# Kernel optimization log

Hardware: AMD Instinct MI355X
Metric: run time of the kernel (lower is better)

Reference implementation:

```python
import jax, jax.numpy as jnp
import numpy as np

DIM, IDIM, HEADS = 256, 64, 4
B, I, J = 1, 256, 256
EPS = 1e-5


def _sinu(seq, rot):
    inv = 1.0 / (10000.0 ** (np.arange(0, rot, 2, dtype=np.float64) / rot))
    f = np.arange(seq, dtype=np.float64)[:, None] * inv[None, :]   # [seq, rot/2]
    f = np.repeat(f, 2, axis=-1)                                   # [seq, rot]
    return (jnp.asarray(np.sin(f)[None], dtype=jnp.float32),
            jnp.asarray(np.cos(f)[None], dtype=jnp.float32))       # [1, seq, rot]


def setup_inputs() -> dict:
    key = jax.random.key(0)
    ks = jax.random.split(key, 8)
    w = DIM ** -0.5
    sin_i, cos_i = _sinu(J, IDIM)
    sin_j, cos_j = _sinu(I, IDIM)
    return {
        'x': jax.random.normal(ks[0], (B, I, J, DIM), jnp.float32),
        'sin_i': sin_i, 'cos_i': cos_i, 'sin_j': sin_j, 'cos_j': cos_j,
        'gia': jnp.ones((DIM,), jnp.float32), 'bia': jnp.zeros((DIM,), jnp.float32),
        'gib': jnp.ones((DIM,), jnp.float32), 'bib': jnp.zeros((DIM,), jnp.float32),
        'Wq_i': jax.random.normal(ks[1], (DIM, IDIM * HEADS), jnp.float32) * w,
        'Wkv_i': jax.random.normal(ks[2], (DIM, 2 * IDIM * HEADS), jnp.float32) * w,
        'Wo_i': jax.random.normal(ks[3], (IDIM * HEADS, DIM), jnp.float32) * w,
        'bo_i': jnp.zeros((DIM,), jnp.float32),
        'gja': jnp.ones((DIM,), jnp.float32), 'bja': jnp.zeros((DIM,), jnp.float32),
        'gjb': jnp.ones((DIM,), jnp.float32), 'bjb': jnp.zeros((DIM,), jnp.float32),
        'Wq_j': jax.random.normal(ks[4], (DIM, IDIM * HEADS), jnp.float32) * w,
        'Wkv_j': jax.random.normal(ks[5], (DIM, 2 * IDIM * HEADS), jnp.float32) * w,
        'Wo_j': jax.random.normal(ks[6], (IDIM * HEADS, DIM), jnp.float32) * w,
        'bo_j': jnp.zeros((DIM,), jnp.float32),
    }


def _ln(x, g, b):
    mu = jnp.mean(x, axis=-1, keepdims=True)
    var = jnp.mean((x - mu) ** 2, axis=-1, keepdims=True)
    return (x - mu) / jnp.sqrt(var + EPS) * g + b


def _rotate_every_two(x):
    x1, x2 = x[..., ::2], x[..., 1::2]
    return jnp.stack((-x2, x1), axis=-1).reshape(x.shape)


def _rope(x, sin, cos):
    # sin/cos: [1, seq, rot] -> [1, 1, seq, rot] (broadcast over heads)
    sin, cos = sin[:, None], cos[:, None]
    rd = sin.shape[-1]
    xr, xp = x[..., :rd], x[..., rd:]
    xr = xr * cos + _rotate_every_two(xr) * sin
    return jnp.concatenate((xr, xp), axis=-1)


def _attn(a, sin, cos, ga, ba, gb, bb, Wq, Wkv, Wo, bo):
    an = _ln(a, ga, ba)
    bn = _ln(a, gb, bb)  # a == b in axial use
    q = an @ Wq
    k, v = jnp.split(bn @ Wkv, 2, axis=-1)
    Bn, N = a.shape[0], a.shape[1]
    def heads(t):
        return t.reshape(Bn, N, HEADS, IDIM).transpose(0, 2, 1, 3)  # b h n d
    q, k, v = heads(q), heads(k), heads(v)
    q = _rope(q, sin, cos)
    k = _rope(k, sin, cos)
    dots = jnp.einsum('bhid,bhjd->bhij', q, k)  # scale = 1 (as in source)
    attn = jax.nn.softmax(dots, axis=-1)
    out = jnp.einsum('bhij,bhjd->bhid', attn, v)
    out = out.transpose(0, 2, 3, 1).reshape(Bn, N, IDIM * HEADS)  # 'b h i d -> b i (d h)'
    return jax.nn.elu(out @ Wo + bo)


def reference(x, sin_i, cos_i, sin_j, cos_j,
              gia, bia, gib, bib, Wq_i, Wkv_i, Wo_i, bo_i,
              gja, bja, gjb, bjb, Wq_j, Wkv_j, Wo_j, bo_j):
    b, i, j, d = x.shape
    xi = x.reshape(b * i, j, d)
    xi = _attn(xi, sin_i, cos_i, gia, bia, gib, bib, Wq_i, Wkv_i, Wo_i, bo_i)
    xi = xi.reshape(b, i, j, d)
    xj = x.transpose(0, 2, 1, 3).reshape(b * j, i, d)
    xj = _attn(xj, sin_j, cos_j, gja, bja, gjb, bjb, Wq_j, Wkv_j, Wo_j, bo_j)
    xj = xj.reshape(b, j, i, d).transpose(0, 2, 1, 3)
    return x + (xi + xj) / 2
```

## Files before the change

### kernel.cpp

```cpp
#include <hip/hip_runtime.h>
#include <math.h>

#define DIM    256
#define IDIM   64
#define HEADS  4
#define NSEQ   256
#define SEQLEN 256
#define NTOK   (NSEQ * SEQLEN)
#define EPSLN  1e-5f

typedef __attribute__((ext_vector_type(8))) short bf16x8s;
typedef __attribute__((ext_vector_type(4))) float f32x4;

union BF8 { bf16x8s v; unsigned short u[8]; };

__device__ __forceinline__ float bf2f(unsigned short u) {
    union { unsigned int i; float f; } v; v.i = ((unsigned int)u) << 16; return v.f;
}
__device__ __forceinline__ unsigned short f2bf(float f) {
    union { float f; unsigned int i; } v; v.f = f;
    unsigned int x = v.i;
    return (unsigned short)((x + 0x7fffu + ((x >> 16) & 1u)) >> 16);
}

__device__ bf16x8s g_wpk[8][8192];

__global__ __launch_bounds__(256) void wpack_all_kernel(
    const float* __restrict__ Wq_i, const float* __restrict__ Wkv_i,
    const float* __restrict__ Wo_i,
    const float* __restrict__ Wq_j, const float* __restrict__ Wkv_j,
    const float* __restrict__ Wo_j)
{
    const int slot = blockIdx.y;
    const int pass = slot >> 2, m = slot & 3;
    const float* W; int ldw, col0, perm;
    if (m == 0)      { W = pass ? Wq_j  : Wq_i;  ldw = 256; col0 = 0;   perm = 0; }
    else if (m == 1) { W = pass ? Wkv_j : Wkv_i; ldw = 512; col0 = 0;   perm = 0; }
    else if (m == 2) { W = pass ? Wkv_j : Wkv_i; ldw = 512; col0 = 256; perm = 0; }
    else             { W = pass ? Wo_j  : Wo_i;  ldw = 256; col0 = 0;   perm = 1; }

    const int gtile = blockIdx.x * 4 + (threadIdx.x >> 6);
    const int l = threadIdx.x & 63;
    const int nt = gtile >> 3, kt = gtile & 7;
    const int n = nt * 16 + (l & 15);
    const int k0 = kt * 32 + (l >> 4) * 8;
    BF8 o;
#pragma unroll
    for (int j = 0; j < 8; ++j) {
        int k = k0 + j;
        int src = perm ? ((k & 63) * 4 + (k >> 6)) : k;
        o.u[j] = f2bf(W[(size_t)src * ldw + col0 + n]);
    }
    g_wpk[slot][(size_t)gtile * 64 + l] = o.v;
}

#define XLD  264
#define GOFF (32 * XLD)
#define CLD2 261

__global__ __launch_bounds__(512) void lnqkv_kernel(
    const float* __restrict__ x,
    const float* __restrict__ sin_t, const float* __restrict__ cos_t,
    const float* __restrict__ ga, const float* __restrict__ ba,
    const float* __restrict__ gb, const float* __restrict__ bb,
    bf16x8s* __restrict__ qo, bf16x8s* __restrict__ ko, bf16x8s* __restrict__ vo,
    int pass)
{
    __shared__ float smf[32 * XLD + 1024];

    const int tid = threadIdx.x;
    const int l = tid & 63, w = tid >> 6;
    const int lr = l & 15, lk = l >> 4;
    const int t0 = blockIdx.x * 32;
    const int seq = t0 >> 8;
    const int pos0 = t0 & 255;
    const int wbase = pass * 4;

    {
        const int half = tid >> 8;
        const int col  = tid & 255;
        for (int rr = 0; rr < 16; ++rr) {
            int r = rr + 16 * half;
            int t = t0 + r;
            int row = (pass == 0) ? t : ((t & 255) * NSEQ + (t >> 8));
            smf[r * XLD + col] = x[(size_t)row * DIM + col];
        }
        smf[GOFF + tid]       = (tid < 256) ? ga[tid] : ba[tid - 256];
        smf[GOFF + 512 + tid] = (tid < 256) ? gb[tid] : bb[tid - 256];
    }
    __syncthreads();

    {
        const int r = tid >> 4, sub = tid & 15;
        float s1 = 0.f, s2 = 0.f;
        for (int m = 0; m < 16; ++m) { float v = smf[r * XLD + sub + 16 * m]; s1 += v; s2 += v * v; }
        for (int off = 1; off < 16; off <<= 1) {
            s1 += __shfl_xor(s1, off, 64);
            s2 += __shfl_xor(s2, off, 64);
        }
        float mu = s1 * (1.f / 256.f);
        float var = s2 * (1.f / 256.f) - mu * mu;
        float rstd = rsqrtf(var + EPSLN);
        for (int m = 0; m < 16; ++m) {
            int d = sub + 16 * m;
            smf[r * XLD + d] = (smf[r * XLD + d] - mu) * rstd;
        }
    }
    __syncthreads();

    f32x4 acc[2][6];
#pragma unroll
    for (int mf = 0; mf < 2; ++mf)
#pragma unroll
        for (int nf = 0; nf < 6; ++nf) { f32x4 z = {0.f, 0.f, 0.f, 0.f}; acc[mf][nf] = z; }

    const int nt0 = w * 6;
    const bool needA = (nt0 < 16);
    const bool needB = (nt0 + 5 >= 16);

    for (int ks = 0; ks < 8; ++ks) {
        const int c0 = ks * 32 + lk * 8;
        if (needA) {
            BF8 ah[2], al[2];
#pragma unroll
            for (int mf = 0; mf < 2; ++mf) {
                const float* xr = &smf[(mf * 16 + lr) * XLD + c0];
                const float* gg = &smf[GOFF + c0];
                const float* bv = &smf[GOFF + 256 + c0];
#pragma unroll
                for (int j = 0; j < 8; ++j) {
                    float a = xr[j] * gg[j] + bv[j];
                    unsigned short hi = f2bf(a);
                    ah[mf].u[j] = hi;
                    al[mf].u[j] = f2bf(a - bf2f(hi));
                }
            }
#pragma unroll
            for (int nf = 0; nf < 6; ++nf) {
                int ntg = nt0 + nf;
                if (ntg < 16) {
                    const bf16x8s b = g_wpk[wbase][((size_t)(ntg * 8 + ks)) * 64 + l];
#pragma unroll
                    for (int mf = 0; mf < 2; ++mf) {
                        acc[mf][nf] = __builtin_amdgcn_mfma_f32_16x16x32_bf16(al[mf].v, b, acc[mf][nf], 0, 0, 0);
                        acc[mf][nf] = __builtin_amdgcn_mfma_f32_16x16x32_bf16(ah[mf].v, b, acc[mf][nf], 0, 0, 0);
                    }
                }
            }
        }
        if (needB) {
            BF8 ah[2], al[2];
#pragma unroll
            for (int mf = 0; mf < 2; ++mf) {
                const float* xr = &smf[(mf * 16 + lr) * XLD + c0];
                const float* gg = &smf[GOFF + 512 + c0];
                const float* bv = &smf[GOFF + 768 + c0];
#pragma unroll
                for (int j = 0; j < 8; ++j) {
                    float a = xr[j] * gg[j] + bv[j];
                    unsigned short hi = f2bf(a);
                    ah[mf].u[j] = hi;
                    al[mf].u[j] = f2bf(a - bf2f(hi));
                }
            }
#pragma unroll
            for (int nf = 0; nf < 6; ++nf) {
                int ntg = nt0 + nf;
                if (ntg >= 16) {
                    const bf16x8s b = g_wpk[wbase + (ntg >> 4)][((size_t)((ntg & 15) * 8 + ks)) * 64 + l];
#pragma unroll
                    for (int mf = 0; mf < 2; ++mf) {
                        acc[mf][nf] = __builtin_amdgcn_mfma_f32_16x16x32_bf16(al[mf].v, b, acc[mf][nf], 0, 0, 0);
                        acc[mf][nf] = __builtin_amdgcn_mfma_f32_16x16x32_bf16(ah[mf].v, b, acc[mf][nf], 0, 0, 0);
                    }
                }
            }
        }
    }
    __syncthreads();

    for (int c = 0; c < 3; ++c) {
#pragma unroll
        for (int nf = 0; nf < 6; ++nf) {
            int ntg = nt0 + nf;
            if ((ntg >> 4) == c) {
                int cb = (ntg & 15) * 16 + lr;
#pragma unroll
                for (int mf = 0; mf < 2; ++mf)
#pragma unroll
                    for (int r = 0; r < 4; ++r)
                        smf[(mf * 16 + lk * 4 + r) * CLD2 + cb] = acc[mf][nf][r];
            }
        }
        __syncthreads();

        if (c < 2) {
#pragma unroll
            for (int p = 0; p < 2; ++p) {
                int tile = w * 2 + p;
                int h = tile >> 2, mt = (tile >> 1) & 1, ktd = tile & 1;
                int row = mt * 16 + lr;
                int pos = pos0 + row;
                int d0 = ktd * 32 + lk * 8;
                const float* src = &smf[row * CLD2 + h * 64 + d0];
                BF8 o;
#pragma unroll
                for (int p2 = 0; p2 < 4; ++p2) {
                    float cs = cos_t[pos * IDIM + d0 + 2 * p2];
                    float sn = sin_t[pos * IDIM + d0 + 2 * p2];
                    float e = src[2 * p2], od = src[2 * p2 + 1];
                    o.u[2 * p2]     = f2bf(e * cs - od * sn);
                    o.u[2 * p2 + 1] = f2bf(od * cs + e * sn);
                }
                int sh = seq * 4 + h;
                int mtg = (pos0 >> 4) + mt;
                bf16x8s* dst = c ? ko : qo;
                dst[((size_t)sh * 32 + mtg * 2 + ktd) * 64 + l] = o.v;
            }
        } else {
#pragma unroll
            for (int p = 0; p < 2; ++p) {
                int tile = w * 2 + p;
                int h = tile >> 2, ntd = tile & 3;
                BF8 o;
#pragma unroll
                for (int j = 0; j < 8; ++j)
                    o.u[j] = f2bf(smf[(lk * 8 + j) * CLD2 + h * 64 + ntd * 16 + lr]);
                int sh = seq * 4 + h;
                int ktg = pos0 >> 5;
                vo[((size_t)sh * 32 + ktg * 4 + ntd) * 64 + l] = o.v;
            }
        }
        __syncthreads();
    }
}

__global__ __launch_bounds__(256) void attn_kernel(
    const bf16x8s* __restrict__ qpk, const bf16x8s* __restrict__ kpk,
    const bf16x8s* __restrict__ vpk, bf16x8s* __restrict__ opk)
{
    __shared__ __align__(16) unsigned short Pus[4 * 64 * 64];
    char* Pb = (char*)Pus;
    const int tid = threadIdx.x, l = tid & 63, w = tid >> 6;
    const int lr = l & 15, lk = l >> 4;
    const int sh = blockIdx.x;
    const size_t base = (size_t)sh * 32 * 64;

    bf16x8s qf[4][2];
#pragma unroll
    for (int mf = 0; mf < 4; ++mf)
#pragma unroll
        for (int kt = 0; kt < 2; ++kt)
            qf[mf][kt] = qpk[base + ((size_t)((w * 4 + mf) * 2 + kt)) * 64 + l];

    f32x4 O[4][4];
    float mrun[4][4], lrun[4][4];
#pragma unroll
    for (int mf = 0; mf < 4; ++mf)
#pragma unroll
        for (int nf = 0; nf < 4; ++nf) { f32x4 z = {0.f, 0.f, 0.f, 0.f}; O[mf][nf] = z; }
#pragma unroll
    for (int mf = 0; mf < 4; ++mf)
#pragma unroll
        for (int r = 0; r < 4; ++r) { mrun[mf][r] = -1e30f; lrun[mf][r] = 0.f; }

    for (int ktk = 0; ktk < 4; ++ktk) {
        f32x4 S[4][4];
#pragma unroll
        for (int mf = 0; mf < 4; ++mf)
#pragma unroll
            for (int nf = 0; nf < 4; ++nf) { f32x4 z = {0.f, 0.f, 0.f, 0.f}; S[mf][nf] = z; }
#pragma unroll
        for (int ks = 0; ks < 2; ++ks) {
            bf16x8s kf[4];
#pragma unroll
            for (int nf = 0; nf < 4; ++nf)
                kf[nf] = kpk[base + ((size_t)((ktk * 4 + nf) * 2 + ks)) * 64 + l];
#pragma unroll
            for (int mf = 0; mf < 4; ++mf)
#pragma unroll
                for (int nf = 0; nf < 4; ++nf)
                    S[mf][nf] = __builtin_amdgcn_mfma_f32_16x16x32_bf16(qf[mf][ks], kf[nf], S[mf][nf], 0, 0, 0);
        }
#pragma unroll
        for (int mf = 0; mf < 4; ++mf) {
#pragma unroll
            for (int r = 0; r < 4; ++r) {
                float mt_ = fmaxf(fmaxf(S[mf][0][r], S[mf][1][r]), fmaxf(S[mf][2][r], S[mf][3][r]));
                for (int off = 1; off < 16; off <<= 1) mt_ = fmaxf(mt_, __shfl_xor(mt_, off, 64));
                float mnew = fmaxf(mrun[mf][r], mt_);
                float sc = __expf(mrun[mf][r] - mnew);
#pragma unroll
                for (int nf = 0; nf < 4; ++nf) O[mf][nf][r] *= sc;
                float ps = 0.f;
#pragma unroll
                for (int nf = 0; nf < 4; ++nf) {
                    float pp = __expf(S[mf][nf][r] - mnew);
                    S[mf][nf][r] = pp;
                    ps += pp;
                }
                for (int off = 1; off < 16; off <<= 1) ps += __shfl_xor(ps, off, 64);
                lrun[mf][r] = lrun[mf][r] * sc + ps;
                mrun[mf][r] = mnew;
            }
        }
#pragma unroll
        for (int mf = 0; mf < 4; ++mf)
#pragma unroll
            for (int nf = 0; nf < 4; ++nf)
#pragma unroll
                for (int r = 0; r < 4; ++r) {
                    int row = mf * 16 + lk * 4 + r, col = nf * 16 + lr;
                    unsigned int byte = ((unsigned)((w * 64 + row) * 64 + col) * 2) ^ (unsigned)((row & 7) << 4);
                    *(unsigned short*)(Pb + byte) = f2bf(S[mf][nf][r]);
                }
        __syncthreads();
#pragma unroll
        for (int ks = 0; ks < 2; ++ks) {
            bf16x8s vf[4];
#pragma unroll
            for (int nf = 0; nf < 4; ++nf)
                vf[nf] = vpk[base + ((size_t)((ktk * 2 + ks) * 4 + nf)) * 64 + l];
#pragma unroll
            for (int mf = 0; mf < 4; ++mf) {
                int row = mf * 16 + lr;
                unsigned int byte = ((unsigned)((w * 64 + row) * 64 + ks * 32 + lk * 8) * 2) ^ (unsigned)((row & 7) << 4);
                bf16x8s pa = *(const bf16x8s*)(Pb + byte);
#pragma unroll
                for (int nf = 0; nf < 4; ++nf)
                    O[mf][nf] = __builtin_amdgcn_mfma_f32_16x16x32_bf16(pa, vf[nf], O[mf][nf], 0, 0, 0);
            }
        }
        __syncthreads();
    }

#pragma unroll
    for (int mf = 0; mf < 4; ++mf)
#pragma unroll
        for (int r = 0; r < 4; ++r) {
            float inv = 1.f / lrun[mf][r];
#pragma unroll
            for (int nf = 0; nf < 4; ++nf) {
                int row = mf * 16 + lk * 4 + r, col = nf * 16 + lr;
                unsigned int byte = ((unsigned)((w * 64 + row) * 64 + col) * 2) ^ (unsigned)((row & 7) << 4);
                *(unsigned short*)(Pb + byte) = f2bf(O[mf][nf][r] * inv);
            }
        }
    __syncthreads();
    const int seq = sh >> 2, h = sh & 3;
#pragma unroll
    for (int mf = 0; mf < 4; ++mf)
#pragma unroll
        for (int ktd = 0; ktd < 2; ++ktd) {
            int row = mf * 16 + lr;
            unsigned int byte = ((unsigned)((w * 64 + row) * 64 + ktd * 32 + lk * 8) * 2) ^ (unsigned)((row & 7) << 4);
            bf16x8s o = *(const bf16x8s*)(Pb + byte);
            size_t mtg = (size_t)seq * 16 + w * 4 + mf;
            opk[(mtg * 8 + h * 2 + ktd) * 64 + l] = o;
        }
}

__device__ __forceinline__ void gemm_core(
    const bf16x8s* __restrict__ A, const bf16x8s* __restrict__ B,
    int mt0, int nt0, int l, f32x4 acc[4][4])
{
#pragma unroll
    for (int mf = 0; mf < 4; ++mf)
#pragma unroll
        for (int nf = 0; nf < 4; ++nf) { f32x4 z = {0.f, 0.f, 0.f, 0.f}; acc[mf][nf] = z; }
#pragma unroll
    for (int ks = 0; ks < 8; ++ks) {
        bf16x8s a[4], b[4];
#pragma unroll
        for (int mf = 0; mf < 4; ++mf) a[mf] = A[((size_t)(mt0 + mf) * 8 + ks) * 64 + l];
#pragma unroll
        for (int nf = 0; nf < 4; ++nf) b[nf] = B[((size_t)(nt0 + nf) * 8 + ks) * 64 + l];
#pragma unroll
        for (int mf = 0; mf < 4; ++mf)
#pragma unroll
            for (int nf = 0; nf < 4; ++nf)
                acc[mf][nf] = __builtin_amdgcn_mfma_f32_16x16x32_bf16(a[mf], b[nf], acc[mf][nf], 0, 0, 0);
    }
}

__global__ __launch_bounds__(256) void gemm_proj_kernel(
    const bf16x8s* __restrict__ A,
    const float* __restrict__ x, const float* __restrict__ bo,
    float* __restrict__ out, int pass)
{
    __shared__ unsigned short Cus[128][136];
    const int tid = threadIdx.x;
    const int l = tid & 63, w = tid >> 6;
    const int wm = w >> 1, wn = w & 1;
    const int mb = blockIdx.x, nb = blockIdx.y;

    f32x4 acc[4][4];
    gemm_core(A, g_wpk[pass * 4 + 3], mb * 8 + wm * 4, nb * 8 + wn * 4, l, acc);

#pragma unroll
    for (int mf = 0; mf < 4; ++mf)
#pragma unroll
        for (int nf = 0; nf < 4; ++nf)
#pragma unroll
            for (int r = 0; r < 4; ++r)
                Cus[wm * 64 + mf * 16 + (l >> 4) * 4 + r][wn * 64 + nf * 16 + (l & 15)] =
                    f2bf(acc[mf][nf][r]);
    __syncthreads();

    const int row = tid >> 1;
    const int cc0 = (tid & 1) * 64;
    const int tok = mb * 128 + row;
    const size_t prow = (pass == 0) ? (size_t)tok
                                    : ((size_t)(tok & 255) * NSEQ + (tok >> 8));
    const size_t gb = prow * DIM + nb * 128 + cc0;
#pragma unroll
    for (int qq = 0; qq < 16; ++qq) {
        float4 r4;
        const float4 b4 = *reinterpret_cast<const float4*>(&bo[nb * 128 + cc0 + qq * 4]);
        float y0 = bf2f(Cus[row][cc0 + qq * 4 + 0]) + b4.x;
        float y1 = bf2f(Cus[row][cc0 + qq * 4 + 1]) + b4.y;
        float y2 = bf2f(Cus[row][cc0 + qq * 4 + 2]) + b4.z;
        float y3 = bf2f(Cus[row][cc0 + qq * 4 + 3]) + b4.w;
        r4.x = 0.5f * (y0 > 0.f ? y0 : expm1f(y0));
        r4.y = 0.5f * (y1 > 0.f ? y1 : expm1f(y1));
        r4.z = 0.5f * (y2 > 0.f ? y2 : expm1f(y2));
        r4.w = 0.5f * (y3 > 0.f ? y3 : expm1f(y3));
        if (pass == 0) {
            const float4 x4 = *reinterpret_cast<const float4*>(&x[gb + qq * 4]);
            r4.x += x4.x; r4.y += x4.y; r4.z += x4.z; r4.w += x4.w;
            *reinterpret_cast<float4*>(&out[gb + qq * 4]) = r4;
        } else {
            float4* op = reinterpret_cast<float4*>(&out[gb + qq * 4]);
            float4 o4 = *op;
            o4.x += r4.x; o4.y += r4.y; o4.z += r4.z; o4.w += r4.w;
            *op = o4;
        }
    }
}

extern "C" void kernel_launch(void* const* d_in, const int* in_sizes, int n_in,
                              void* d_out, int out_size, void* d_ws, size_t ws_size,
                              hipStream_t stream) {
    const float* x     = (const float*)d_in[0];
    const float* sin_i = (const float*)d_in[1];
    const float* cos_i = (const float*)d_in[2];
    const float* sin_j = (const float*)d_in[3];
    const float* cos_j = (const float*)d_in[4];
    const float* gia   = (const float*)d_in[5];
    const float* bia   = (const float*)d_in[6];
    const float* gib   = (const float*)d_in[7];
    const float* bib   = (const float*)d_in[8];
    const float* Wq_i  = (const float*)d_in[9];
    const float* Wkv_i = (const float*)d_in[10];
    const float* Wo_i  = (const float*)d_in[11];
    const float* bo_i  = (const float*)d_in[12];
    const float* gja   = (const float*)d_in[13];
    const float* bja   = (const float*)d_in[14];
    const float* gjb   = (const float*)d_in[15];
    const float* bjb   = (const float*)d_in[16];
    const float* Wq_j  = (const float*)d_in[17];
    const float* Wkv_j = (const float*)d_in[18];
    const float* Wo_j  = (const float*)d_in[19];
    const float* bo_j  = (const float*)d_in[20];

    float* out = (float*)d_out;

    char* base = (char*)d_ws;
    const size_t MB32 = 33554432;
    bf16x8s* buf0 = (bf16x8s*)(base);
    bf16x8s* buf1 = (bf16x8s*)(base + MB32);
    bf16x8s* buf2 = (bf16x8s*)(base + 2 * MB32);
    bf16x8s* buf3 = (bf16x8s*)(base + 3 * MB32);

    wpack_all_kernel<<<dim3(32, 8), 256, 0, stream>>>(Wq_i, Wkv_i, Wo_i, Wq_j, Wkv_j, Wo_j);

    for (int pass = 0; pass < 2; ++pass) {
        const float* sin_t = pass ? sin_j : sin_i;
        const float* cos_t = pass ? cos_j : cos_i;
        const float* ga = pass ? gja : gia;  const float* ba = pass ? bja : bia;
        const float* gb = pass ? gjb : gib;  const float* bb = pass ? bjb : bib;
        const float* bo = pass ? bo_j : bo_i;

        lnqkv_kernel<<<2048, 512, 0, stream>>>(
            x, sin_t, cos_t, ga, ba, gb, bb, buf2, buf3, buf0, pass);
        attn_kernel<<<1024, 256, 0, stream>>>(buf2, buf3, buf0, buf1);
        gemm_proj_kernel<<<dim3(512, 2), 256, 0, stream>>>(buf1, x, bo, out, pass);
    }
}
```

Before: 638.9 us.

## Fold LayerNorm affine into QKV weights and precompute bf16 hi/lo split once

Folds the LayerNorm gamma into the packed Q/KV weights and turns beta into a per-column bias (beta·W), computed once by a new small kernel and added in the epilogue. The normalized activations are split into bf16 hi/lo once per element and stored in shared memory, so the GEMM inner loop does vector LDS loads instead of per-fragment affine math and conversions. The two code paths for the A and B normalizations also merge into one. The trade-offs are an extra tiny kernel launch and a slightly different rounding order, since gamma is rounded into the bf16 weights.

```diff
diff --git a/kernel.cpp b/kernel.cpp
--- a/kernel.cpp
+++ b/kernel.cpp
@@ -24,20 +24,24 @@
 }
 
 __device__ bf16x8s g_wpk[8][8192];
+__device__ float g_bias[8][256];
 
 __global__ __launch_bounds__(256) void wpack_all_kernel(
     const float* __restrict__ Wq_i, const float* __restrict__ Wkv_i,
     const float* __restrict__ Wo_i,
     const float* __restrict__ Wq_j, const float* __restrict__ Wkv_j,
-    const float* __restrict__ Wo_j)
+    const float* __restrict__ Wo_j,
+    const float* __restrict__ gia, const float* __restrict__ gib,
+    const float* __restrict__ gja, const float* __restrict__ gjb)
 {
     const int slot = blockIdx.y;
     const int pass = slot >> 2, m = slot & 3;
     const float* W; int ldw, col0, perm;
-    if (m == 0)      { W = pass ? Wq_j  : Wq_i;  ldw = 256; col0 = 0;   perm = 0; }
-    else if (m == 1) { W = pass ? Wkv_j : Wkv_i; ldw = 512; col0 = 0;   perm = 0; }
-    else if (m == 2) { W = pass ? Wkv_j : Wkv_i; ldw = 512; col0 = 256; perm = 0; }
-    else             { W = pass ? Wo_j  : Wo_i;  ldw = 256; col0 = 0;   perm = 1; }
+    const float* gam;
+    if (m == 0)      { W = pass ? Wq_j  : Wq_i;  ldw = 256; col0 = 0;   perm = 0; gam = pass ? gja : gia; }
+    else if (m == 1) { W = pass ? Wkv_j : Wkv_i; ldw = 512; col0 = 0;   perm = 0; gam = pass ? gjb : gib; }
+    else if (m == 2) { W = pass ? Wkv_j : Wkv_i; ldw = 512; col0 = 256; perm = 0; gam = pass ? gjb : gib; }
+    else             { W = pass ? Wo_j  : Wo_i;  ldw = 256; col0 = 0;   perm = 1; gam = 0; }
 
     const int gtile = blockIdx.x * 4 + (threadIdx.x >> 6);
     const int l = threadIdx.x & 63;
@@ -49,24 +53,44 @@
     for (int j = 0; j < 8; ++j) {
         int k = k0 + j;
         int src = perm ? ((k & 63) * 4 + (k >> 6)) : k;
-        o.u[j] = f2bf(W[(size_t)src * ldw + col0 + n]);
+        float wv = W[(size_t)src * ldw + col0 + n];
+        if (gam) wv *= gam[k];
+        o.u[j] = f2bf(wv);
     }
     g_wpk[slot][(size_t)gtile * 64 + l] = o.v;
 }
 
+__global__ __launch_bounds__(256) void bias_kernel(
+    const float* __restrict__ bia, const float* __restrict__ bib,
+    const float* __restrict__ bja, const float* __restrict__ bjb,
+    const float* __restrict__ Wq_i, const float* __restrict__ Wkv_i,
+    const float* __restrict__ Wq_j, const float* __restrict__ Wkv_j)
+{
+    const int s = blockIdx.x;
+    const int pass = s / 3, m = s % 3;
+    const float* beta = (m == 0) ? (pass ? bja : bia) : (pass ? bjb : bib);
+    const float* W    = (m == 0) ? (pass ? Wq_j : Wq_i) : (pass ? Wkv_j : Wkv_i);
+    const int ldw  = (m == 0) ? 256 : 512;
+    const int col0 = (m == 2) ? 256 : 0;
+    const int col  = threadIdx.x;
+    float acc = 0.f;
+    for (int k = 0; k < 256; ++k) acc += beta[k] * W[(size_t)k * ldw + col0 + col];
+    g_bias[pass * 4 + m][col] = acc;
+}
+
 #define XLD  264
-#define GOFF (32 * XLD)
+#define HLD  264
 #define CLD2 261
 
 __global__ __launch_bounds__(512) void lnqkv_kernel(
     const float* __restrict__ x,
     const float* __restrict__ sin_t, const float* __restrict__ cos_t,
-    const float* __restrict__ ga, const float* __restrict__ ba,
-    const float* __restrict__ gb, const float* __restrict__ bb,
     bf16x8s* __restrict__ qo, bf16x8s* __restrict__ ko, bf16x8s* __restrict__ vo,
     int pass)
 {
-    __shared__ float smf[32 * XLD + 1024];
+    __shared__ __align__(16) float smf[16896];
+    unsigned short* hi = (unsigned short*)(smf + 8448);
+    unsigned short* lo = (unsigned short*)(smf + 8448 + 4224);
 
     const int tid = threadIdx.x;
     const int l = tid & 63, w = tid >> 6;
@@ -85,8 +109,6 @@
             int row = (pass == 0) ? t : ((t & 255) * NSEQ + (t >> 8));
             smf[r * XLD + col] = x[(size_t)row * DIM + col];
         }
-        smf[GOFF + tid]       = (tid < 256) ? ga[tid] : ba[tid - 256];
-        smf[GOFF + 512 + tid] = (tid < 256) ? gb[tid] : bb[tid - 256];
     }
     __syncthreads();
 
@@ -103,7 +125,11 @@
         float rstd = rsqrtf(var + EPSLN);
         for (int m = 0; m < 16; ++m) {
             int d = sub + 16 * m;
-            smf[r * XLD + d] = (smf[r * XLD + d] - mu) * rstd;
+            float v = (smf[r * XLD + d] - mu) * rstd;
+            union { float f; unsigned int u; } a; a.f = v;
+            unsigned short h = (unsigned short)(a.u >> 16);
+            hi[r * HLD + d] = h;
+            lo[r * HLD + d] = f2bf(v - bf2f(h));
         }
     }
     __syncthreads();
@@ -115,65 +141,23 @@
         for (int nf = 0; nf < 6; ++nf) { f32x4 z = {0.f, 0.f, 0.f, 0.f}; acc[mf][nf] = z; }
 
     const int nt0 = w * 6;
-    const bool needA = (nt0 < 16);
-    const bool needB = (nt0 + 5 >= 16);
-
     for (int ks = 0; ks < 8; ++ks) {
         const int c0 = ks * 32 + lk * 8;
-        if (needA) {
-            BF8 ah[2], al[2];
+        bf16x8s ahi[2], alo[2];
+#pragma unroll
+        for (int mf = 0; mf < 2; ++mf) {
+            const int row = mf * 16 + lr;
+            ahi[mf] = *(const bf16x8s*)(hi + row * HLD + c0);
+            alo[mf] = *(const bf16x8s*)(lo + row * HLD + c0);
+        }
+#pragma unroll
+        for (int nf = 0; nf < 6; ++nf) {
+            const int ntg = nt0 + nf;
+            const bf16x8s b = g_wpk[wbase + (ntg >> 4)][((size_t)((ntg & 15) * 8 + ks)) * 64 + l];
 #pragma unroll
             for (int mf = 0; mf < 2; ++mf) {
-                const float* xr = &smf[(mf * 16 + lr) * XLD + c0];
-                const float* gg = &smf[GOFF + c0];
-                const float* bv = &smf[GOFF + 256 + c0];
-#pragma unroll
-                for (int j = 0; j < 8; ++j) {
-                    float a = xr[j] * gg[j] + bv[j];
-                    unsigned short hi = f2bf(a);
-                    ah[mf].u[j] = hi;
-                    al[mf].u[j] = f2bf(a - bf2f(hi));
-                }
-            }
-#pragma unroll
-            for (int nf = 0; nf < 6; ++nf) {
-                int ntg = nt0 + nf;
-                if (ntg < 16) {
-                    const bf16x8s b = g_wpk[wbase][((size_t)(ntg * 8 + ks)) * 64 + l];
-#pragma unroll
-                    for (int mf = 0; mf < 2; ++mf) {
-                        acc[mf][nf] = __builtin_amdgcn_mfma_f32_16x16x32_bf16(al[mf].v, b, acc[mf][nf], 0, 0, 0);
-                        acc[mf][nf] = __builtin_amdgcn_mfma_f32_16x16x32_bf16(ah[mf].v, b, acc[mf][nf], 0, 0, 0);
-                    }
-                }
-            }
-        }
-        if (needB) {
-            BF8 ah[2], al[2];
-#pragma unroll
-            for (int mf = 0; mf < 2; ++mf) {
-                const float* xr = &smf[(mf * 16 + lr) * XLD + c0];
-                const float* gg = &smf[GOFF + 512 + c0];
-                const float* bv = &smf[GOFF + 768 + c0];
-#pragma unroll
-                for (int j = 0; j < 8; ++j) {
-                    float a = xr[j] * gg[j] + bv[j];
-                    unsigned short hi = f2bf(a);
-                    ah[mf].u[j] = hi;
-                    al[mf].u[j] = f2bf(a - bf2f(hi));
-                }
-            }
-#pragma unroll
-            for (int nf = 0; nf < 6; ++nf) {
-                int ntg = nt0 + nf;
-                if (ntg >= 16) {
-                    const bf16x8s b = g_wpk[wbase + (ntg >> 4)][((size_t)((ntg & 15) * 8 + ks)) * 64 + l];
-#pragma unroll
-                    for (int mf = 0; mf < 2; ++mf) {
-                        acc[mf][nf] = __builtin_amdgcn_mfma_f32_16x16x32_bf16(al[mf].v, b, acc[mf][nf], 0, 0, 0);
-                        acc[mf][nf] = __builtin_amdgcn_mfma_f32_16x16x32_bf16(ah[mf].v, b, acc[mf][nf], 0, 0, 0);
-                    }
-                }
+                acc[mf][nf] = __builtin_amdgcn_mfma_f32_16x16x32_bf16(alo[mf], b, acc[mf][nf], 0, 0, 0);
+                acc[mf][nf] = __builtin_amdgcn_mfma_f32_16x16x32_bf16(ahi[mf], b, acc[mf][nf], 0, 0, 0);
             }
         }
     }
@@ -203,12 +187,14 @@
                 int pos = pos0 + row;
                 int d0 = ktd * 32 + lk * 8;
                 const float* src = &smf[row * CLD2 + h * 64 + d0];
+                const float* bv = &g_bias[wbase + c][h * 64 + d0];
                 BF8 o;
 #pragma unroll
                 for (int p2 = 0; p2 < 4; ++p2) {
                     float cs = cos_t[pos * IDIM + d0 + 2 * p2];
                     float sn = sin_t[pos * IDIM + d0 + 2 * p2];
-                    float e = src[2 * p2], od = src[2 * p2 + 1];
+                    float e  = src[2 * p2]     + bv[2 * p2];
+                    float od = src[2 * p2 + 1] + bv[2 * p2 + 1];
                     o.u[2 * p2]     = f2bf(e * cs - od * sn);
                     o.u[2 * p2 + 1] = f2bf(od * cs + e * sn);
                 }
@@ -222,10 +208,12 @@
             for (int p = 0; p < 2; ++p) {
                 int tile = w * 2 + p;
                 int h = tile >> 2, ntd = tile & 3;
+                int col = h * 64 + ntd * 16 + lr;
+                float bb_ = g_bias[wbase + 2][col];
                 BF8 o;
 #pragma unroll
                 for (int j = 0; j < 8; ++j)
-                    o.u[j] = f2bf(smf[(lk * 8 + j) * CLD2 + h * 64 + ntd * 16 + lr]);
+                    o.u[j] = f2bf(smf[(lk * 8 + j) * CLD2 + col] + bb_);
                 int sh = seq * 4 + h;
                 int ktg = pos0 >> 5;
                 vo[((size_t)sh * 32 + ktg * 4 + ntd) * 64 + l] = o.v;
@@ -472,17 +460,18 @@
     bf16x8s* buf2 = (bf16x8s*)(base + 2 * MB32);
     bf16x8s* buf3 = (bf16x8s*)(base + 3 * MB32);
 
-    wpack_all_kernel<<<dim3(32, 8), 256, 0, stream>>>(Wq_i, Wkv_i, Wo_i, Wq_j, Wkv_j, Wo_j);
+    wpack_all_kernel<<<dim3(32, 8), 256, 0, stream>>>(
+        Wq_i, Wkv_i, Wo_i, Wq_j, Wkv_j, Wo_j, gia, gib, gja, gjb);
+    bias_kernel<<<6, 256, 0, stream>>>(
+        bia, bib, bja, bjb, Wq_i, Wkv_i, Wq_j, Wkv_j);
 
     for (int pass = 0; pass < 2; ++pass) {
         const float* sin_t = pass ? sin_j : sin_i;
         const float* cos_t = pass ? cos_j : cos_i;
-        const float* ga = pass ? gja : gia;  const float* ba = pass ? bja : bia;
-        const float* gb = pass ? gjb : gib;  const float* bb = pass ? bjb : bib;
         const float* bo = pass ? bo_j : bo_i;
 
         lnqkv_kernel<<<2048, 512, 0, stream>>>(
-            x, sin_t, cos_t, ga, ba, gb, bb, buf2, buf3, buf0, pass);
+            x, sin_t, cos_t, buf2, buf3, buf0, pass);
         attn_kernel<<<1024, 256, 0, stream>>>(buf2, buf3, buf0, buf1);
         gemm_proj_kernel<<<dim3(512, 2), 256, 0, stream>>>(buf1, x, bo, out, pass);
     }
```

Result: slower. 749.5 us (+17.3%).
